# Kernel tuning notes

Measured on AMD Instinct MI355X. Metric: run time of the kernel, lower is better.

Reference implementation:

```python
import jax, jax.numpy as jnp
import numpy as np

B, S, DIM, E, K = 8, 8192, 512, 4, 2
EPS = 1e-6


def setup_inputs() -> dict:
    key = jax.random.key(0)
    ks = jax.random.split(key, 4)
    scale = 0.02
    return {
        "x": jax.random.normal(ks[0], (B, S, DIM), dtype=jnp.float32),
        "router_w": jax.random.normal(ks[1], (DIM, E), dtype=jnp.float32) * scale,
        "router_b": jnp.zeros((E,), jnp.float32),
        "expert_w": jax.random.normal(ks[2], (E, DIM, DIM), dtype=jnp.float32) * scale,
        "expert_b": jnp.zeros((E, DIM), jnp.float32),
        "out_w": jax.random.normal(ks[3], (DIM, DIM), dtype=jnp.float32) * scale,
        "out_b": jnp.zeros((DIM,), jnp.float32),
        "norm_w": jnp.ones((DIM,), jnp.float32),
    }


def reference(x, router_w, router_b, expert_w, expert_b, out_w, out_b, norm_w):
    b, s, d = x.shape
    # router
    logits = x @ router_w + router_b                      # [B,S,E]
    topw, topi = jax.lax.top_k(logits, K)                 # [B,S,K]
    topw = jax.nn.softmax(topw, axis=-1)
    t = b * s
    xf = x.reshape(t, d)
    idx = topi.reshape(t, K)
    w = topw.reshape(t, K).astype(x.dtype)
    # dense token-expert weight mask (topk indices are distinct per token)
    mask = jnp.zeros((t, E), x.dtype).at[jnp.arange(t)[:, None], idx].set(w)
    # expert FFN: Linear + SiLU (dropout disabled in eval)
    h = jax.nn.silu(jnp.einsum("td,edh->teh", xf, expert_w) + expert_b)  # [T,E,D]
    comb = jnp.einsum("te,teh->th", mask, h)              # weighted combine
    out = comb @ out_w + out_b
    y = xf + out                                          # residual
    rms = jnp.sqrt(jnp.mean(y * y, axis=-1, keepdims=True) + EPS)
    return (norm_w * (y / rms)).reshape(b, s, d)
```

## Files before the change

### kernel.cpp

```cpp
#include <hip/hip_runtime.h>
#include <hip/hip_bf16.h>
#include <stdint.h>

#define NTOK 65536
#define DIM 512
#define NEXP 4
#define REG 14336

using u16 = unsigned short;
using u32 = unsigned int;
typedef __attribute__((ext_vector_type(4))) float f32x4;
typedef __attribute__((ext_vector_type(8))) short bf16x8;
typedef __attribute__((ext_vector_type(8))) u16 u16x8;
typedef __attribute__((ext_vector_type(4))) u16 u16x4;

__device__ __forceinline__ u16 f2bf(float f) {
  u32 u = __builtin_bit_cast(u32, f);
  u32 r = (u + 0x7FFFu + ((u >> 16) & 1u)) >> 16;
  return (u16)r;
}
__device__ __forceinline__ float bf2f(u16 v) {
  return __builtin_bit_cast(float, (u32)v << 16);
}

#define GLOAD_LDS16(gp, lp)                                                    \
  __builtin_amdgcn_global_load_lds(                                            \
      (const __attribute__((address_space(1))) void*)(gp),                     \
      (__attribute__((address_space(3))) void*)(lp), 16, 0, 0)

#define FENCE asm volatile("" ::: "memory")
#define BARRIER { FENCE; __builtin_amdgcn_s_barrier(); FENCE; }
#define LGKM0 { asm volatile("s_waitcnt lgkmcnt(0)" ::: "memory"); __builtin_amdgcn_sched_barrier(0); }
#define VMCNT_(n) asm volatile("s_waitcnt vmcnt(" #n ")" ::: "memory")
#define VMCNT(n) VMCNT_(n)
#define SB __builtin_amdgcn_sched_barrier(0)

__device__ __forceinline__ const bf16x8* lds_frag(const u16* base, int row, int chunk) {
  return (const bf16x8*)((const char*)base + row * 128 + (((chunk) ^ (row & 7)) << 4));
}

__global__ void packw(const float* __restrict__ ew, const float* __restrict__ ow,
                      u16* __restrict__ ewtp, u16* __restrict__ owt3,
                      int* __restrict__ cnt) {
  if (blockIdx.x == 0 && threadIdx.x < 6) cnt[threadIdx.x] = 0;
  int lane = threadIdx.x & 63, wv = threadIdx.x >> 6;
  int gf = blockIdx.x * 4 + wv;
  int r16 = lane & 15, lg = lane >> 4;
  u16x8 o;
  if (gf < 2048) {
    int hs = gf & 31, T = (gf >> 5) & 15, e = gf >> 9;
    int h = hs * 16 + r16;
    int d0 = T * 32 + lg * 8;
#pragma unroll
    for (int q = 0; q < 8; ++q)
      o[q] = f2bf(ew[((size_t)e * DIM + d0 + q) * DIM + h]);
    *(u16x8*)(ewtp + (size_t)gf * 512 + lane * 8) = o;
  } else {
    int frag = gf - 2048;
    int j = frag & 7, kc = (frag >> 3) & 1, t = (frag >> 4) & 7, strip = frag >> 7;
    int h = strip * 128 + j * 16 + r16;
    int d0 = t * 64 + kc * 32 + lg * 8;
#pragma unroll
    for (int q = 0; q < 8; ++q) o[q] = f2bf(ow[(size_t)(d0 + q) * DIM + h]);
    *(u16x8*)(owt3 + (size_t)frag * 512 + lane * 8) = o;
  }
}

__global__ void router_kernel(const float* __restrict__ x, const float* __restrict__ rw,
                              const float* __restrict__ rb, u16* __restrict__ xb,
                              int* __restrict__ pp, float2* __restrict__ wab) {
  int lane = threadIdx.x & 63, wave = threadIdx.x >> 6;
  size_t t = (size_t)blockIdx.x * 4 + wave;
  const float* xr = x + t * DIM + lane * 8;
  f32x4 v0 = *(const f32x4*)xr;
  f32x4 v1 = *(const f32x4*)(xr + 4);
  float l0 = 0.f, l1 = 0.f, l2 = 0.f, l3 = 0.f;
  const float* rwp = rw + (size_t)lane * 32;
#pragma unroll
  for (int j = 0; j < 8; ++j) {
    float xv = (j < 4) ? v0[j] : v1[j - 4];
    f32x4 r = *(const f32x4*)(rwp + j * 4);
    l0 += xv * r[0]; l1 += xv * r[1]; l2 += xv * r[2]; l3 += xv * r[3];
  }
#pragma unroll
  for (int off = 32; off; off >>= 1) {
    l0 += __shfl_xor(l0, off); l1 += __shfl_xor(l1, off);
    l2 += __shfl_xor(l2, off); l3 += __shfl_xor(l3, off);
  }
  float lv[4] = {l0 + rb[0], l1 + rb[1], l2 + rb[2], l3 + rb[3]};
  int i0 = 0; float b0 = lv[0];
#pragma unroll
  for (int e = 1; e < 4; ++e) if (lv[e] > b0) { b0 = lv[e]; i0 = e; }
  int i1 = (i0 == 0) ? 1 : 0; float b1 = lv[i1];
#pragma unroll
  for (int e = 0; e < 4; ++e) if (e != i0 && lv[e] > b1) { b1 = lv[e]; i1 = e; }
  float ex = __expf(b1 - b0);
  float w0 = 1.0f / (1.0f + ex);
  float w1 = ex * w0;
  if (lane == 0) {
    int a = (i0 < i1) ? i0 : i1;
    int b = (i0 < i1) ? i1 : i0;
    const int ptab[16] = {-1, 0, 1, 2, -1, -1, 3, 4, -1, -1, -1, 5, -1, -1, -1, -1};
    pp[t] = ptab[a * 4 + b];
    float wa = (a == i0) ? w0 : w1;
    float wb = (a == i0) ? w1 : w0;
    wab[t] = make_float2(wa, wb);
  }
  u16x8 o;
#pragma unroll
  for (int j = 0; j < 4; ++j) { o[j] = f2bf(v0[j]); o[4 + j] = f2bf(v1[j]); }
  *(u16x8*)(xb + t * DIM + lane * 8) = o;
}

__global__ void assignscatter(const int* __restrict__ pp, const float2* __restrict__ wab,
                              int* __restrict__ cnt, int* __restrict__ list,
                              float2* __restrict__ wpair) {
  int t = blockIdx.x * 256 + threadIdx.x;
  int lane = threadIdx.x & 63;
  int p = pp[t];
  float2 w = wab[t];
  int pos = 0;
#pragma unroll
  for (int q = 0; q < 6; ++q) {
    unsigned long long m = __ballot(p == q);
    if (p == q) {
      int rank = __popcll(m & ((1ull << lane) - 1ull));
      int leader = __ffsll((long long)m) - 1;
      int base = 0;
      if (lane == leader) base = atomicAdd(&cnt[q], (int)__popcll(m));
      base = __shfl(base, leader);
      pos = base + rank;
    }
  }
  int slot = p * REG + pos;
  if (pos < REG) {
    list[slot] = t;
    wpair[slot] = w;
  }
}

__global__ __launch_bounds__(256, 2) void expert_gemm(
    const u16* __restrict__ xb, const u16* __restrict__ ewtp,
    const float* __restrict__ ebias, const int* __restrict__ cnt,
    const int* __restrict__ list, const float2* __restrict__ wpair,
    u16* __restrict__ comb) {
  __shared__ u16 Asl[3][128 * 64];
  int tid = threadIdx.x, lane = tid & 63, wave = tid >> 6;
  int wy = wave >> 1, wx = wave & 1;
  int b = blockIdx.x;
  int chunk = b >> 5, within = b & 31;
  int panel = chunk * 8 + (within & 7);
  int nblk = within >> 3;
  int p = panel / (REG / 128);
  int m0 = panel * 128;
  int cntp = cnt[p];
  if (m0 - p * REG >= cntp) return;
  int n0 = nblk * 128;
  const int ea2[6] = {0, 0, 0, 1, 1, 2};
  const int eb2[6] = {1, 2, 3, 2, 3, 3};
  int eA = ea2[p], eB = eb2[p];

  int r16 = lane & 15, lg = lane >> 4;
  int rl = lane >> 3;
  int scb = ((lane & 7) ^ rl) * 8;
  int s = r16 & 7;
  int ab0 = (wy * 64 + r16) * 128 + ((s >> 2) << 6) + ((lg ^ (s & 3)) << 4);
  int ab1 = ab0 ^ 64;

  int sid[4];
#pragma unroll
  for (int j = 0; j < 4; ++j) {
    int slot = m0 + wave * 32 + j * 8 + rl;
    int idv = list[slot];
    sid[j] = ((slot - p * REG) < cntp) ? idv : 0;
  }
  const u16* a0b = xb + (size_t)sid[0] * DIM + scb;
  const u16* a1b = xb + (size_t)sid[1] * DIM + scb;
  const u16* a2b = xb + (size_t)sid[2] * DIM + scb;
  const u16* a3b = xb + (size_t)sid[3] * DIM + scb;
  const u16* bpA = ewtp + (size_t)eA * 262144 + (size_t)(n0 / 16 + wx * 4) * 512 + lane * 8;
  const u16* bpB = ewtp + (size_t)eB * 262144 + (size_t)(n0 / 16 + wx * 4) * 512 + lane * 8;

  f32x4 accA[4][4], accB[4][4];
#pragma unroll
  for (int i = 0; i < 4; ++i)
#pragma unroll
    for (int j = 0; j < 4; ++j) { accA[i][j] = (f32x4)(0.f); accB[i][j] = (f32x4)(0.f); }

#define STAGE(BI, KS)                                                          \
  do {                                                                         \
    GLOAD_LDS16(a0b + (KS) * 64, Asl[BI] + (wave * 32) * 64);                  \
    GLOAD_LDS16(a1b + (KS) * 64, Asl[BI] + (wave * 32 + 8) * 64);              \
    GLOAD_LDS16(a2b + (KS) * 64, Asl[BI] + (wave * 32 + 16) * 64);             \
    GLOAD_LDS16(a3b + (KS) * 64, Asl[BI] + (wave * 32 + 24) * 64);             \
  } while (0)
#define LOADB(BV, T32)                                                         \
  do {                                                                         \
    _Pragma("unroll") for (int i = 0; i < 4; ++i) {                            \
      BV[i]     = *(const bf16x8*)(bpA + (T32) * 16384 + i * 512);             \
      BV[4 + i] = *(const bf16x8*)(bpB + (T32) * 16384 + i * 512);             \
    }                                                                          \
  } while (0)

  STAGE(0, 0); SB;
  STAGE(1, 1); SB;
  VMCNT(4);
  BARRIER;

  bf16x8 Bk0[8], Bk1[8];
#define KST(T, WC)                                                             \
  {                                                                            \
    LOADB(Bk0, 2 * (T));                                                       \
    LOADB(Bk1, 2 * (T) + 1);                                                   \
    SB;                                                                        \
    if ((T) + 2 < 8) { STAGE(((T) + 2) % 3, (T) + 2); }                        \
    SB;                                                                        \
    const char* Ab_ = (const char*)Asl[(T) % 3];                               \
    bf16x8 a[4];                                                               \
    _Pragma("unroll") for (int i = 0; i < 4; ++i)                              \
      a[i] = *(const bf16x8*)(Ab_ + ab0 + i * 2048);                           \
    __builtin_amdgcn_s_setprio(1);                                             \
    _Pragma("unroll") for (int i = 0; i < 4; ++i)                              \
      _Pragma("unroll") for (int j = 0; j < 4; ++j)                            \
        accA[i][j] = __builtin_amdgcn_mfma_f32_16x16x32_bf16(a[i], Bk0[j], accA[i][j], 0, 0, 0); \
    _Pragma("unroll") for (int i = 0; i < 4; ++i)                              \
      _Pragma("unroll") for (int j = 0; j < 4; ++j)                            \
        accB[i][j] = __builtin_amdgcn_mfma_f32_16x16x32_bf16(a[i], Bk0[4 + j], accB[i][j], 0, 0, 0); \
    __builtin_amdgcn_s_setprio(0);                                             \
    _Pragma("unroll") for (int i = 0; i < 4; ++i)                              \
      a[i] = *(const bf16x8*)(Ab_ + ab1 + i * 2048);                           \
    __builtin_amdgcn_s_setprio(1);                                             \
    _Pragma("unroll") for (int i = 0; i < 4; ++i)                              \
      _Pragma("unroll") for (int j = 0; j < 4; ++j)                            \
        accA[i][j] = __builtin_amdgcn_mfma_f32_16x16x32_bf16(a[i], Bk1[j], accA[i][j], 0, 0, 0); \
    _Pragma("unroll") for (int i = 0; i < 4; ++i)                              \
      _Pragma("unroll") for (int j = 0; j < 4; ++j)                            \
        accB[i][j] = __builtin_amdgcn_mfma_f32_16x16x32_bf16(a[i], Bk1[4 + j], accB[i][j], 0, 0, 0); \
    __builtin_amdgcn_s_setprio(0);                                             \
    WC;                                                                        \
  }

  KST(0, { VMCNT(4); BARRIER; })
  KST(1, { VMCNT(4); BARRIER; })
  KST(2, { VMCNT(4); BARRIER; })
  KST(3, { VMCNT(4); BARRIER; })
  KST(4, { VMCNT(4); BARRIER; })
  KST(5, { VMCNT(4); BARRIER; })
  KST(6, { VMCNT(0); BARRIER; })
  KST(7, {})
#undef KST
#undef LOADB
#undef STAGE

  float bA4[4], bB4[4];
#pragma unroll
  for (int j = 0; j < 4; ++j) {
    int h = n0 + wx * 64 + j * 16 + r16;
    bA4[j] = ebias[eA * DIM + h];
    bB4[j] = ebias[eB * DIM + h];
  }
#pragma unroll
  for (int i = 0; i < 4; ++i) {
    int rb = wy * 64 + i * 16 + lg * 4;
#pragma unroll
    for (int rr = 0; rr < 4; ++rr) {
      int slot = m0 + rb + rr;
      bool val = (slot - p * REG) < cntp;
      int id = list[slot];
      float2 wv = wpair[slot];
#pragma unroll
      for (int j = 0; j < 4; ++j) {
        float zA = accA[i][j][rr] + bA4[j];
        float zB = accB[i][j][rr] + bB4[j];
        float sA = zA / (1.0f + __expf(-zA));
        float sB = zB / (1.0f + __expf(-zB));
        float v = wv.x * sA + wv.y * sB;
        if (val) {
          int h = n0 + wx * 64 + j * 16 + r16;
          comb[(size_t)id * DIM + h] = f2bf(v);
        }
      }
    }
  }
}

__global__ __launch_bounds__(256, 2) void outnorm(
    const u16* __restrict__ comb, const u16* __restrict__ owt3,
    const float* __restrict__ ob, const u16* __restrict__ xb,
    const float* __restrict__ nw, float* __restrict__ out) {
  __shared__ u16 As[3][64 * 64];
  __shared__ float rowsum[64][4];
  int tid = threadIdx.x, lane = tid & 63, w = tid >> 6;
  int m0 = blockIdx.x * 64;
  int r16 = lane & 15, lg = lane >> 4;
  int rl = lane >> 3;
  int scb = ((lane & 7) ^ rl) * 8;
  int n0w = w * 128;

  f32x4 acc[8][4];
#pragma unroll
  for (int j = 0; j < 8; ++j)
#pragma unroll
    for (int i = 0; i < 4; ++i) acc[j][i] = (f32x4)(0.f);

#define OSTG(bi, ks)                                                           \
  _Pragma("unroll") for (int jj = 0; jj < 2; ++jj) {                           \
    GLOAD_LDS16(comb + (size_t)(m0 + w * 16 + jj * 8 + rl) * DIM + (ks) * 64 + scb, \
                As[bi] + (w * 16 + jj * 8) * 64);                              \
  }
#define LOADB(BV, HH)                                                          \
  {                                                                            \
    const u16* bp_ = owt3 +                                                    \
        ((size_t)(((w * 8 + ((HH) >> 1)) * 2 + ((HH) & 1)) * 8)) * 512 + lane * 8; \
    _Pragma("unroll") for (int jj = 0; jj < 8; ++jj)                           \
      BV[jj] = *(const bf16x8*)(bp_ + jj * 512);                               \
  }
#define HSTEP(H, BC, BN, WC)                                                   \
  {                                                                            \
    if (((H) & 1) == 0 && ((H) >> 1) + 2 < 8) OSTG((((H) >> 1) + 2) % 3, ((H) >> 1) + 2); \
    if ((H) + 1 < 16) LOADB(BN, (H) + 1);                                      \
    bf16x8 af[4];                                                              \
    _Pragma("unroll") for (int ii = 0; ii < 4; ++ii)                           \
      af[ii] = *lds_frag(As[((H) >> 1) % 3], ii * 16 + r16, ((H) & 1) * 4 + lg); \
    LGKM0;                                                                     \
    __builtin_amdgcn_s_setprio(1);                                             \
    _Pragma("unroll") for (int jj = 0; jj < 8; ++jj)                           \
      _Pragma("unroll") for (int ii = 0; ii < 4; ++ii)                         \
        acc[jj][ii] = __builtin_amdgcn_mfma_f32_16x16x32_bf16(BC[jj], af[ii], acc[jj][ii], 0, 0, 0); \
    __builtin_amdgcn_s_setprio(0);                                             \
    WC;                                                                        \
  }

  bf16x8 BE[8], BO[8];
  OSTG(0, 0); OSTG(1, 1);
  LOADB(BE, 0);
  VMCNT(10);
  BARRIER;

  HSTEP(0,  BE, BO, {})
  HSTEP(1,  BO, BE, { VMCNT(10); BARRIER; })
  HSTEP(2,  BE, BO, {})
  HSTEP(3,  BO, BE, { VMCNT(10); BARRIER; })
  HSTEP(4,  BE, BO, {})
  HSTEP(5,  BO, BE, { VMCNT(10); BARRIER; })
  HSTEP(6,  BE, BO, {})
  HSTEP(7,  BO, BE, { VMCNT(10); BARRIER; })
  HSTEP(8,  BE, BO, {})
  HSTEP(9,  BO, BE, { VMCNT(10); BARRIER; })
  HSTEP(10, BE, BO, {})
  HSTEP(11, BO, BE, { VMCNT(10); BARRIER; })
  HSTEP(12, BE, BO, {})
  HSTEP(13, BO, BE, { VMCNT(8); BARRIER; })
  HSTEP(14, BE, BO, {})
  HSTEP(15, BO, BE, {})
#undef HSTEP
#undef LOADB
#undef OSTG

  float part[4] = {0.f, 0.f, 0.f, 0.f};
#pragma unroll
  for (int hj = 0; hj < 8; ++hj) {
    int h0 = n0w + hj * 16 + lg * 4;
    f32x4 obv = *(const f32x4*)(ob + h0);
#pragma unroll
    for (int ti = 0; ti < 4; ++ti) {
      int t = m0 + ti * 16 + r16;
      u16x4 xv4 = *(const u16x4*)(xb + (size_t)t * DIM + h0);
#pragma unroll
      for (int rr = 0; rr < 4; ++rr) {
        float yv = bf2f(xv4[rr]) + acc[hj][ti][rr] + obv[rr];
        acc[hj][ti][rr] = yv;
        part[ti] += yv * yv;
      }
    }
  }
#pragma unroll
  for (int ti = 0; ti < 4; ++ti) {
    part[ti] += __shfl_xor(part[ti], 16);
    part[ti] += __shfl_xor(part[ti], 32);
  }
  if (lane < 16) {
#pragma unroll
    for (int ti = 0; ti < 4; ++ti) rowsum[ti * 16 + r16][w] = part[ti];
  }
  __syncthreads();
  float inv[4];
#pragma unroll
  for (int ti = 0; ti < 4; ++ti) {
    int tr = ti * 16 + r16;
    float s = rowsum[tr][0] + rowsum[tr][1] + rowsum[tr][2] + rowsum[tr][3];
    inv[ti] = 1.0f / sqrtf(s * (1.0f / 512.0f) + 1e-6f);
  }
#pragma unroll
  for (int hj = 0; hj < 8; ++hj) {
    int h0 = n0w + hj * 16 + lg * 4;
    f32x4 nwv = *(const f32x4*)(nw + h0);
#pragma unroll
    for (int ti = 0; ti < 4; ++ti) {
      int t = m0 + ti * 16 + r16;
      f32x4 o;
#pragma unroll
      for (int rr = 0; rr < 4; ++rr) o[rr] = acc[hj][ti][rr] * inv[ti] * nwv[rr];
      *(f32x4*)(out + (size_t)t * DIM + h0) = o;
    }
  }
}

extern "C" void kernel_launch(void* const* d_in, const int* in_sizes, int n_in,
                              void* d_out, int out_size, void* d_ws, size_t ws_size,
                              hipStream_t stream) {
  const float* x  = (const float*)d_in[0];
  const float* rw = (const float*)d_in[1];
  const float* rb = (const float*)d_in[2];
  const float* ew = (const float*)d_in[3];
  const float* eb = (const float*)d_in[4];
  const float* ow = (const float*)d_in[5];
  const float* ob = (const float*)d_in[6];
  const float* nw = (const float*)d_in[7];
  float* out = (float*)d_out;

  char* ws = (char*)d_ws;
  u16*   xb    = (u16*)(ws);
  u16*   combb = (u16*)(ws + 67108864);
  int*   pp    = (int*)(ws + 67108864);
  float2* wab  = (float2*)(ws + 67108864 + 262144);
  u16*   ewtp  = (u16*)(ws + 134217728);
  u16*   owt3  = (u16*)(ws + 136314880);
  int*   list  = (int*)(ws + 136839168);
  float2* wpair = (float2*)(ws + 136839168 + 344064);
  int*   cnt   = (int*)(ws + 136839168 + 344064 + 688128);

  packw<<<640, 256, 0, stream>>>(ew, ow, ewtp, owt3, cnt);
  router_kernel<<<NTOK / 4, 256, 0, stream>>>(x, rw, rb, xb, pp, wab);
  assignscatter<<<NTOK / 256, 256, 0, stream>>>(pp, wab, cnt, list, wpair);
  expert_gemm<<<dim3(6 * REG / 128 * 4), 256, 0, stream>>>(xb, ewtp, eb, cnt, list, wpair, combb);
  outnorm<<<dim3(NTOK / 64), 256, 0, stream>>>(combb, owt3, ob, xb, nw, out);
}
```

Before: 317.8 us.

## Fuse expert GEMM and output projection with RMSNorm into one kernel

Merges the expert FFN GEMM and the output projection plus residual RMSNorm into a single kernel. Each 512-thread block owns a 64-token panel across the full 512 hidden width. The combined activations stay in swizzled LDS instead of a global bf16 buffer, and results are scattered straight back to token rows. This removes the global write and read of the comb tensor and one launch. The cost is that each block now reloads the full expert and output weights, the tile is smaller with one block per CU, and the output rows are written scattered.

```diff
diff --git a/kernel.cpp b/kernel.cpp
--- a/kernel.cpp
+++ b/kernel.cpp
@@ -30,14 +30,9 @@
 
 #define FENCE asm volatile("" ::: "memory")
 #define BARRIER { FENCE; __builtin_amdgcn_s_barrier(); FENCE; }
-#define LGKM0 { asm volatile("s_waitcnt lgkmcnt(0)" ::: "memory"); __builtin_amdgcn_sched_barrier(0); }
 #define VMCNT_(n) asm volatile("s_waitcnt vmcnt(" #n ")" ::: "memory")
 #define VMCNT(n) VMCNT_(n)
 #define SB __builtin_amdgcn_sched_barrier(0)
-
-__device__ __forceinline__ const bf16x8* lds_frag(const u16* base, int row, int chunk) {
-  return (const bf16x8*)((const char*)base + row * 128 + (((chunk) ^ (row & 7)) << 4));
-}
 
 __global__ void packw(const float* __restrict__ ew, const float* __restrict__ ow,
                       u16* __restrict__ ewtp, u16* __restrict__ owt3,
@@ -139,47 +134,38 @@
   }
 }
 
-__global__ __launch_bounds__(256, 2) void expert_gemm(
+__global__ __launch_bounds__(512, 1) void moe_fused(
     const u16* __restrict__ xb, const u16* __restrict__ ewtp,
-    const float* __restrict__ ebias, const int* __restrict__ cnt,
-    const int* __restrict__ list, const float2* __restrict__ wpair,
-    u16* __restrict__ comb) {
-  __shared__ u16 Asl[3][128 * 64];
-  int tid = threadIdx.x, lane = tid & 63, wave = tid >> 6;
-  int wy = wave >> 1, wx = wave & 1;
-  int b = blockIdx.x;
-  int chunk = b >> 5, within = b & 31;
-  int panel = chunk * 8 + (within & 7);
-  int nblk = within >> 3;
-  int p = panel / (REG / 128);
-  int m0 = panel * 128;
+    const u16* __restrict__ owt3, const float* __restrict__ ebias,
+    const float* __restrict__ ob, const float* __restrict__ nw,
+    const int* __restrict__ cnt, const int* __restrict__ list,
+    const float2* __restrict__ wpair, float* __restrict__ out) {
+  __shared__ char smem[24576 + 65536];
+  u16* AslBase = (u16*)smem;
+  u16* comb = (u16*)(smem + 24576);
+  float* rowsum = (float*)smem;
+
+  int tid = threadIdx.x, lane = tid & 63, w = tid >> 6;
+  int r16 = lane & 15, lg = lane >> 4;
+  int rl = lane >> 3;
+  int scb = ((lane & 7) ^ rl) * 8;
+  int w8 = w * 8;
+
+  int panel = blockIdx.x;
+  int p = panel / (REG / 64);
+  int m0 = panel * 64;
   int cntp = cnt[p];
   if (m0 - p * REG >= cntp) return;
-  int n0 = nblk * 128;
   const int ea2[6] = {0, 0, 0, 1, 1, 2};
   const int eb2[6] = {1, 2, 3, 2, 3, 3};
   int eA = ea2[p], eB = eb2[p];
 
-  int r16 = lane & 15, lg = lane >> 4;
-  int rl = lane >> 3;
-  int scb = ((lane & 7) ^ rl) * 8;
-  int s = r16 & 7;
-  int ab0 = (wy * 64 + r16) * 128 + ((s >> 2) << 6) + ((lg ^ (s & 3)) << 4);
-  int ab1 = ab0 ^ 64;
-
-  int sid[4];
-#pragma unroll
-  for (int j = 0; j < 4; ++j) {
-    int slot = m0 + wave * 32 + j * 8 + rl;
-    int idv = list[slot];
-    sid[j] = ((slot - p * REG) < cntp) ? idv : 0;
-  }
-  const u16* a0b = xb + (size_t)sid[0] * DIM + scb;
-  const u16* a1b = xb + (size_t)sid[1] * DIM + scb;
-  const u16* a2b = xb + (size_t)sid[2] * DIM + scb;
-  const u16* a3b = xb + (size_t)sid[3] * DIM + scb;
-  const u16* bpA = ewtp + (size_t)eA * 262144 + (size_t)(n0 / 16 + wx * 4) * 512 + lane * 8;
-  const u16* bpB = ewtp + (size_t)eB * 262144 + (size_t)(n0 / 16 + wx * 4) * 512 + lane * 8;
+  int slotA = m0 + w8 + rl;
+  int idvA = list[slotA];
+  int sidA = ((slotA - p * REG) < cntp) ? idvA : 0;
+  const u16* abase = xb + (size_t)sidA * DIM + scb;
+  const u16* bpA = ewtp + (size_t)eA * 262144 + (size_t)(w * 4) * 512 + lane * 8;
+  const u16* bpB = ewtp + (size_t)eB * 262144 + (size_t)(w * 4) * 512 + lane * 8;
 
   f32x4 accA[4][4], accB[4][4];
 #pragma unroll
@@ -187,14 +173,8 @@
 #pragma unroll
     for (int j = 0; j < 4; ++j) { accA[i][j] = (f32x4)(0.f); accB[i][j] = (f32x4)(0.f); }
 
-#define STAGE(BI, KS)                                                          \
-  do {                                                                         \
-    GLOAD_LDS16(a0b + (KS) * 64, Asl[BI] + (wave * 32) * 64);                  \
-    GLOAD_LDS16(a1b + (KS) * 64, Asl[BI] + (wave * 32 + 8) * 64);              \
-    GLOAD_LDS16(a2b + (KS) * 64, Asl[BI] + (wave * 32 + 16) * 64);             \
-    GLOAD_LDS16(a3b + (KS) * 64, Asl[BI] + (wave * 32 + 24) * 64);             \
-  } while (0)
-#define LOADB(BV, T32)                                                         \
+#define P1STAGE(BI, KS) GLOAD_LDS16(abase + (KS) * 64, AslBase + (BI) * 4096 + w8 * 64)
+#define P1LOADB(BV, T32)                                                       \
   do {                                                                         \
     _Pragma("unroll") for (int i = 0; i < 4; ++i) {                            \
       BV[i]     = *(const bf16x8*)(bpA + (T32) * 16384 + i * 512);             \
@@ -202,174 +182,129 @@
     }                                                                          \
   } while (0)
 
-  STAGE(0, 0); SB;
-  STAGE(1, 1); SB;
-  VMCNT(4);
+  P1STAGE(0, 0); SB;
+  P1STAGE(1, 1); SB;
+  VMCNT(1);
   BARRIER;
 
   bf16x8 Bk0[8], Bk1[8];
-#define KST(T, WC)                                                             \
+  int sxr = r16 & 7;
+#define KST1(T, WC)                                                            \
   {                                                                            \
-    LOADB(Bk0, 2 * (T));                                                       \
-    LOADB(Bk1, 2 * (T) + 1);                                                   \
+    P1LOADB(Bk0, 2 * (T));                                                     \
+    P1LOADB(Bk1, 2 * (T) + 1);                                                 \
     SB;                                                                        \
-    if ((T) + 2 < 8) { STAGE(((T) + 2) % 3, (T) + 2); }                        \
+    if ((T) + 2 < 8) { P1STAGE(((T) + 2) % 3, (T) + 2); }                      \
     SB;                                                                        \
-    const char* Ab_ = (const char*)Asl[(T) % 3];                               \
+    const char* Ab_ = smem + ((T) % 3) * 8192;                                 \
     bf16x8 a[4];                                                               \
-    _Pragma("unroll") for (int i = 0; i < 4; ++i)                              \
-      a[i] = *(const bf16x8*)(Ab_ + ab0 + i * 2048);                           \
+    _Pragma("unroll") for (int ti = 0; ti < 4; ++ti)                           \
+      a[ti] = *(const bf16x8*)(Ab_ + (ti * 16 + r16) * 128 + ((lg ^ sxr) << 4)); \
     __builtin_amdgcn_s_setprio(1);                                             \
-    _Pragma("unroll") for (int i = 0; i < 4; ++i)                              \
-      _Pragma("unroll") for (int j = 0; j < 4; ++j)                            \
-        accA[i][j] = __builtin_amdgcn_mfma_f32_16x16x32_bf16(a[i], Bk0[j], accA[i][j], 0, 0, 0); \
-    _Pragma("unroll") for (int i = 0; i < 4; ++i)                              \
-      _Pragma("unroll") for (int j = 0; j < 4; ++j)                            \
-        accB[i][j] = __builtin_amdgcn_mfma_f32_16x16x32_bf16(a[i], Bk0[4 + j], accB[i][j], 0, 0, 0); \
+    _Pragma("unroll") for (int hj = 0; hj < 4; ++hj)                           \
+      _Pragma("unroll") for (int ti = 0; ti < 4; ++ti) {                       \
+        accA[hj][ti] = __builtin_amdgcn_mfma_f32_16x16x32_bf16(Bk0[hj], a[ti], accA[hj][ti], 0, 0, 0); \
+        accB[hj][ti] = __builtin_amdgcn_mfma_f32_16x16x32_bf16(Bk0[4 + hj], a[ti], accB[hj][ti], 0, 0, 0); \
+      }                                                                        \
     __builtin_amdgcn_s_setprio(0);                                             \
-    _Pragma("unroll") for (int i = 0; i < 4; ++i)                              \
-      a[i] = *(const bf16x8*)(Ab_ + ab1 + i * 2048);                           \
+    _Pragma("unroll") for (int ti = 0; ti < 4; ++ti)                           \
+      a[ti] = *(const bf16x8*)(Ab_ + (ti * 16 + r16) * 128 + (((4 + lg) ^ sxr) << 4)); \
     __builtin_amdgcn_s_setprio(1);                                             \
-    _Pragma("unroll") for (int i = 0; i < 4; ++i)                              \
-      _Pragma("unroll") for (int j = 0; j < 4; ++j)                            \
-        accA[i][j] = __builtin_amdgcn_mfma_f32_16x16x32_bf16(a[i], Bk1[j], accA[i][j], 0, 0, 0); \
-    _Pragma("unroll") for (int i = 0; i < 4; ++i)                              \
-      _Pragma("unroll") for (int j = 0; j < 4; ++j)                            \
-        accB[i][j] = __builtin_amdgcn_mfma_f32_16x16x32_bf16(a[i], Bk1[4 + j], accB[i][j], 0, 0, 0); \
+    _Pragma("unroll") for (int hj = 0; hj < 4; ++hj)                           \
+      _Pragma("unroll") for (int ti = 0; ti < 4; ++ti) {                       \
+        accA[hj][ti] = __builtin_amdgcn_mfma_f32_16x16x32_bf16(Bk1[hj], a[ti], accA[hj][ti], 0, 0, 0); \
+        accB[hj][ti] = __builtin_amdgcn_mfma_f32_16x16x32_bf16(Bk1[4 + hj], a[ti], accB[hj][ti], 0, 0, 0); \
+      }                                                                        \
     __builtin_amdgcn_s_setprio(0);                                             \
     WC;                                                                        \
   }
 
-  KST(0, { VMCNT(4); BARRIER; })
-  KST(1, { VMCNT(4); BARRIER; })
-  KST(2, { VMCNT(4); BARRIER; })
-  KST(3, { VMCNT(4); BARRIER; })
-  KST(4, { VMCNT(4); BARRIER; })
-  KST(5, { VMCNT(4); BARRIER; })
-  KST(6, { VMCNT(0); BARRIER; })
-  KST(7, {})
-#undef KST
-#undef LOADB
-#undef STAGE
-
-  float bA4[4], bB4[4];
-#pragma unroll
-  for (int j = 0; j < 4; ++j) {
-    int h = n0 + wx * 64 + j * 16 + r16;
-    bA4[j] = ebias[eA * DIM + h];
-    bB4[j] = ebias[eB * DIM + h];
-  }
-#pragma unroll
-  for (int i = 0; i < 4; ++i) {
-    int rb = wy * 64 + i * 16 + lg * 4;
-#pragma unroll
-    for (int rr = 0; rr < 4; ++rr) {
-      int slot = m0 + rb + rr;
-      bool val = (slot - p * REG) < cntp;
-      int id = list[slot];
-      float2 wv = wpair[slot];
-#pragma unroll
-      for (int j = 0; j < 4; ++j) {
-        float zA = accA[i][j][rr] + bA4[j];
-        float zB = accB[i][j][rr] + bB4[j];
-        float sA = zA / (1.0f + __expf(-zA));
-        float sB = zB / (1.0f + __expf(-zB));
-        float v = wv.x * sA + wv.y * sB;
-        if (val) {
-          int h = n0 + wx * 64 + j * 16 + r16;
-          comb[(size_t)id * DIM + h] = f2bf(v);
+  KST1(0, { VMCNT(1); BARRIER; })
+  KST1(1, { VMCNT(1); BARRIER; })
+  KST1(2, { VMCNT(1); BARRIER; })
+  KST1(3, { VMCNT(1); BARRIER; })
+  KST1(4, { VMCNT(1); BARRIER; })
+  KST1(5, { VMCNT(1); BARRIER; })
+  KST1(6, { VMCNT(0); BARRIER; })
+  KST1(7, {})
+#undef KST1
+#undef P1LOADB
+#undef P1STAGE
+
+  {
+    float2 wv[4];
+#pragma unroll
+    for (int ti = 0; ti < 4; ++ti) wv[ti] = wpair[m0 + ti * 16 + r16];
+#pragma unroll
+    for (int hj = 0; hj < 4; ++hj) {
+      int h0 = w * 64 + hj * 16 + lg * 4;
+      f32x4 bA = *(const f32x4*)(ebias + eA * DIM + h0);
+      f32x4 bB = *(const f32x4*)(ebias + eB * DIM + h0);
+      int chunk = h0 >> 3;
+      int inoff = (h0 * 2) & 15;
+#pragma unroll
+      for (int ti = 0; ti < 4; ++ti) {
+        int token = ti * 16 + r16;
+        u16x4 pk;
+#pragma unroll
+        for (int rr = 0; rr < 4; ++rr) {
+          float zA = accA[hj][ti][rr] + bA[rr];
+          float zB = accB[hj][ti][rr] + bB[rr];
+          float sA = zA / (1.0f + __expf(-zA));
+          float sB = zB / (1.0f + __expf(-zB));
+          pk[rr] = f2bf(wv[ti].x * sA + wv[ti].y * sB);
         }
+        *(u16x4*)((char*)comb + token * 1024 + ((chunk ^ (token & 7)) << 4) + inoff) = pk;
       }
     }
   }
-}
-
-__global__ __launch_bounds__(256, 2) void outnorm(
-    const u16* __restrict__ comb, const u16* __restrict__ owt3,
-    const float* __restrict__ ob, const u16* __restrict__ xb,
-    const float* __restrict__ nw, float* __restrict__ out) {
-  __shared__ u16 As[3][64 * 64];
-  __shared__ float rowsum[64][4];
-  int tid = threadIdx.x, lane = tid & 63, w = tid >> 6;
-  int m0 = blockIdx.x * 64;
-  int r16 = lane & 15, lg = lane >> 4;
-  int rl = lane >> 3;
-  int scb = ((lane & 7) ^ rl) * 8;
-  int n0w = w * 128;
-
-  f32x4 acc[8][4];
-#pragma unroll
-  for (int j = 0; j < 8; ++j)
-#pragma unroll
-    for (int i = 0; i < 4; ++i) acc[j][i] = (f32x4)(0.f);
-
-#define OSTG(bi, ks)                                                           \
-  _Pragma("unroll") for (int jj = 0; jj < 2; ++jj) {                           \
-    GLOAD_LDS16(comb + (size_t)(m0 + w * 16 + jj * 8 + rl) * DIM + (ks) * 64 + scb, \
-                As[bi] + (w * 16 + jj * 8) * 64);                              \
-  }
-#define LOADB(BV, HH)                                                          \
-  {                                                                            \
-    const u16* bp_ = owt3 +                                                    \
-        ((size_t)(((w * 8 + ((HH) >> 1)) * 2 + ((HH) & 1)) * 8)) * 512 + lane * 8; \
-    _Pragma("unroll") for (int jj = 0; jj < 8; ++jj)                           \
-      BV[jj] = *(const bf16x8*)(bp_ + jj * 512);                               \
-  }
-#define HSTEP(H, BC, BN, WC)                                                   \
-  {                                                                            \
-    if (((H) & 1) == 0 && ((H) >> 1) + 2 < 8) OSTG((((H) >> 1) + 2) % 3, ((H) >> 1) + 2); \
-    if ((H) + 1 < 16) LOADB(BN, (H) + 1);                                      \
-    bf16x8 af[4];                                                              \
-    _Pragma("unroll") for (int ii = 0; ii < 4; ++ii)                           \
-      af[ii] = *lds_frag(As[((H) >> 1) % 3], ii * 16 + r16, ((H) & 1) * 4 + lg); \
-    LGKM0;                                                                     \
-    __builtin_amdgcn_s_setprio(1);                                             \
-    _Pragma("unroll") for (int jj = 0; jj < 8; ++jj)                           \
-      _Pragma("unroll") for (int ii = 0; ii < 4; ++ii)                         \
-        acc[jj][ii] = __builtin_amdgcn_mfma_f32_16x16x32_bf16(BC[jj], af[ii], acc[jj][ii], 0, 0, 0); \
-    __builtin_amdgcn_s_setprio(0);                                             \
-    WC;                                                                        \
-  }
-
-  bf16x8 BE[8], BO[8];
-  OSTG(0, 0); OSTG(1, 1);
-  LOADB(BE, 0);
-  VMCNT(10);
-  BARRIER;
-
-  HSTEP(0,  BE, BO, {})
-  HSTEP(1,  BO, BE, { VMCNT(10); BARRIER; })
-  HSTEP(2,  BE, BO, {})
-  HSTEP(3,  BO, BE, { VMCNT(10); BARRIER; })
-  HSTEP(4,  BE, BO, {})
-  HSTEP(5,  BO, BE, { VMCNT(10); BARRIER; })
-  HSTEP(6,  BE, BO, {})
-  HSTEP(7,  BO, BE, { VMCNT(10); BARRIER; })
-  HSTEP(8,  BE, BO, {})
-  HSTEP(9,  BO, BE, { VMCNT(10); BARRIER; })
-  HSTEP(10, BE, BO, {})
-  HSTEP(11, BO, BE, { VMCNT(10); BARRIER; })
-  HSTEP(12, BE, BO, {})
-  HSTEP(13, BO, BE, { VMCNT(8); BARRIER; })
-  HSTEP(14, BE, BO, {})
-  HSTEP(15, BO, BE, {})
-#undef HSTEP
-#undef LOADB
-#undef OSTG
-
+  __syncthreads();
+
+  f32x4 acc2[4][4];
+#pragma unroll
+  for (int i = 0; i < 4; ++i)
+#pragma unroll
+    for (int j = 0; j < 4; ++j) acc2[i][j] = (f32x4)(0.f);
+  const u16* owb = owt3 + (size_t)((w >> 1) * 128 + (w & 1) * 4) * 512 + lane * 8;
+#pragma unroll
+  for (int t2 = 0; t2 < 16; ++t2) {
+    bf16x8 bw[4];
+#pragma unroll
+    for (int j = 0; j < 4; ++j) bw[j] = *(const bf16x8*)(owb + t2 * 4096 + j * 512);
+    bf16x8 cf[4];
+#pragma unroll
+    for (int ti = 0; ti < 4; ++ti) {
+      int token = ti * 16 + r16;
+      int chunk = t2 * 4 + lg;
+      cf[ti] = *(const bf16x8*)((char*)comb + token * 1024 + ((chunk ^ (r16 & 7)) << 4));
+    }
+#pragma unroll
+    for (int gj = 0; gj < 4; ++gj)
+#pragma unroll
+      for (int ti = 0; ti < 4; ++ti)
+        acc2[gj][ti] = __builtin_amdgcn_mfma_f32_16x16x32_bf16(bw[gj], cf[ti], acc2[gj][ti], 0, 0, 0);
+  }
+
+  int idt[4]; bool val[4];
+#pragma unroll
+  for (int ti = 0; ti < 4; ++ti) {
+    int slot = m0 + ti * 16 + r16;
+    val[ti] = (slot - p * REG) < cntp;
+    int iv = list[slot];
+    idt[ti] = val[ti] ? iv : 0;
+  }
   float part[4] = {0.f, 0.f, 0.f, 0.f};
 #pragma unroll
-  for (int hj = 0; hj < 8; ++hj) {
-    int h0 = n0w + hj * 16 + lg * 4;
-    f32x4 obv = *(const f32x4*)(ob + h0);
+  for (int gj = 0; gj < 4; ++gj) {
+    int g0 = w * 64 + gj * 16 + lg * 4;
+    f32x4 obv = *(const f32x4*)(ob + g0);
 #pragma unroll
     for (int ti = 0; ti < 4; ++ti) {
-      int t = m0 + ti * 16 + r16;
-      u16x4 xv4 = *(const u16x4*)(xb + (size_t)t * DIM + h0);
+      u16x4 xv4 = *(const u16x4*)(xb + (size_t)idt[ti] * DIM + g0);
 #pragma unroll
       for (int rr = 0; rr < 4; ++rr) {
-        float yv = bf2f(xv4[rr]) + acc[hj][ti][rr] + obv[rr];
-        acc[hj][ti][rr] = yv;
+        float yv = bf2f(xv4[rr]) + acc2[gj][ti][rr] + obv[rr];
+        acc2[gj][ti][rr] = yv;
         part[ti] += yv * yv;
       }
     }
@@ -381,27 +316,30 @@
   }
   if (lane < 16) {
 #pragma unroll
-    for (int ti = 0; ti < 4; ++ti) rowsum[ti * 16 + r16][w] = part[ti];
+    for (int ti = 0; ti < 4; ++ti) rowsum[(ti * 16 + r16) * 8 + w] = part[ti];
   }
   __syncthreads();
   float inv[4];
 #pragma unroll
   for (int ti = 0; ti < 4; ++ti) {
     int tr = ti * 16 + r16;
-    float s = rowsum[tr][0] + rowsum[tr][1] + rowsum[tr][2] + rowsum[tr][3];
+    float s = 0.f;
+#pragma unroll
+    for (int q = 0; q < 8; ++q) s += rowsum[tr * 8 + q];
     inv[ti] = 1.0f / sqrtf(s * (1.0f / 512.0f) + 1e-6f);
   }
 #pragma unroll
-  for (int hj = 0; hj < 8; ++hj) {
-    int h0 = n0w + hj * 16 + lg * 4;
-    f32x4 nwv = *(const f32x4*)(nw + h0);
+  for (int gj = 0; gj < 4; ++gj) {
+    int g0 = w * 64 + gj * 16 + lg * 4;
+    f32x4 nwv = *(const f32x4*)(nw + g0);
 #pragma unroll
     for (int ti = 0; ti < 4; ++ti) {
-      int t = m0 + ti * 16 + r16;
-      f32x4 o;
-#pragma unroll
-      for (int rr = 0; rr < 4; ++rr) o[rr] = acc[hj][ti][rr] * inv[ti] * nwv[rr];
-      *(f32x4*)(out + (size_t)t * DIM + h0) = o;
+      if (val[ti]) {
+        f32x4 o;
+#pragma unroll
+        for (int rr = 0; rr < 4; ++rr) o[rr] = acc2[gj][ti][rr] * inv[ti] * nwv[rr];
+        *(f32x4*)(out + (size_t)idt[ti] * DIM + g0) = o;
+      }
     }
   }
 }
@@ -421,7 +359,6 @@
 
   char* ws = (char*)d_ws;
   u16*   xb    = (u16*)(ws);
-  u16*   combb = (u16*)(ws + 67108864);
   int*   pp    = (int*)(ws + 67108864);
   float2* wab  = (float2*)(ws + 67108864 + 262144);
   u16*   ewtp  = (u16*)(ws + 134217728);
@@ -433,6 +370,6 @@
   packw<<<640, 256, 0, stream>>>(ew, ow, ewtp, owt3, cnt);
   router_kernel<<<NTOK / 4, 256, 0, stream>>>(x, rw, rb, xb, pp, wab);
   assignscatter<<<NTOK / 256, 256, 0, stream>>>(pp, wab, cnt, list, wpair);
-  expert_gemm<<<dim3(6 * REG / 128 * 4), 256, 0, stream>>>(xb, ewtp, eb, cnt, list, wpair, combb);
-  outnorm<<<dim3(NTOK / 64), 256, 0, stream>>>(combb, owt3, ob, xb, nw, out);
-}
+  moe_fused<<<dim3(6 * REG / 64), 512, 0, stream>>>(xb, ewtp, owt3, eb, ob, nw,
+                                                    cnt, list, wpair, out);
+}
```

After: 356.1 us. 12.0% more time.
